# Performance work log

Hardware: AMD Instinct MI355X
Metric: run time of the kernel (lower is better)

The kernel has to match this reference:

```python
import jax, jax.numpy as jnp
import numpy as np

DT_SCALER = 1.0 / 24.0
EULER_STEPS = 10   # odeint euler, t in [0,1], step_size=0.1
STEP = 0.1


def setup_inputs() -> dict:
    key = jax.random.key(0)
    ks = jax.random.split(key, 10)
    B, T, D, H = 8192, 100, 16, 32
    Hd = min((H + D) * 2, 50)  # 50
    x = jax.random.normal(ks[0], (B, T, D), dtype=jnp.float32)
    dt = jax.random.uniform(ks[1], (B, T, 2), dtype=jnp.float32)
    # dh MLP: Linear(H+D -> Hd), tanh, Linear(Hd -> H), tanh ; init N(0, 0.1), bias 0
    W1 = 0.1 * jax.random.normal(ks[2], (Hd, H + D), dtype=jnp.float32)
    b1 = jnp.zeros((Hd,), jnp.float32)
    W2 = 0.1 * jax.random.normal(ks[3], (H, Hd), dtype=jnp.float32)
    b2 = jnp.zeros((H,), jnp.float32)
    # dy MLP: Linear(H -> 2H), tanh, Linear(2H -> 1)
    W3 = 0.1 * jax.random.normal(ks[4], (2 * H, H), dtype=jnp.float32)
    b3 = jnp.zeros((2 * H,), jnp.float32)
    W4 = 0.1 * jax.random.normal(ks[5], (1, 2 * H), dtype=jnp.float32)
    b4 = jnp.zeros((1,), jnp.float32)
    return {"dt": dt, "x": x, "W1": W1, "b1": b1, "W2": W2, "b2": b2,
            "W3": W3, "b3": b3, "W4": W4, "b4": b4}


def _forward(dt, x, W1, b1, W2, b2, W3, b3, W4, b4):
    B, T, D = x.shape
    H = W2.shape[0]
    dti = (dt[:, :, 1] - dt[:, :, 0])[..., None]  # [B,T,1]
    x_t = jnp.swapaxes(x, 0, 1)      # [T,B,D]
    dt_t = jnp.swapaxes(dti, 0, 1)   # [T,B,1]

    def time_step(h, inp):
        x_i, dt_i = inp              # [B,D], [B,1]
        y = x_i[:, 0:1]              # z0 y-part reset to observation each step
        scale = dt_i * DT_SCALER     # [B,1]

        def euler(carry, _):
            y, h = carry
            dh = jnp.tanh(jnp.tanh(jnp.concatenate([x_i, h], axis=1) @ W1.T + b1) @ W2.T + b2) * scale
            dy = (jnp.tanh(h @ W3.T + b3) @ W4.T + b4) * scale
            return (y + STEP * dy, h + STEP * dh), None

        (y, h), _ = jax.lax.scan(euler, (y, h), None, length=EULER_STEPS)
        return h, y

    h0 = jnp.zeros((B, H), jnp.float32)
    _, mu = jax.lax.scan(time_step, h0, (x_t, dt_t))  # mu: [T,B,1]
    return jnp.swapaxes(mu, 0, 1)                     # [B,T,1]


def reference(dt, x, W1, b1, W2, b2, W3, b3, W4, b4):
    return _forward(dt, x, W1, b1, W2, b2, W3, b3, W4, b4)
```

## Files before the change

### kernel.cpp

```cpp
#include <hip/hip_runtime.h>
#include <stdint.h>

#define T_STEPS 100
#define D_IN 16
#define H_DIM 32
#define HD 50
#define KXH 48
#define EULER 10
#define STEPF 0.1f
#define DT_SCALERF (1.0f/24.0f)
#define TANH_SCALE 2.8853900817779268f

typedef __attribute__((ext_vector_type(8))) short short8;
typedef __attribute__((ext_vector_type(4))) float float4v;
typedef __attribute__((ext_vector_type(4))) uint32_t uint4v;

__device__ __forceinline__ float tanh_pre(float us) {
    float e = __builtin_amdgcn_exp2f(us);
    return 1.0f - 2.0f * __builtin_amdgcn_rcpf(e + 1.0f);
}
__device__ __forceinline__ uint32_t pkbf(float lo, float hi) {
    uint32_t r;
    asm("v_cvt_pk_bf16_f32 %0, %1, %2" : "=v"(r) : "v"(lo), "v"(hi));
    return r;
}
__device__ __forceinline__ short f2bf(float f) {
    uint32_t u = __builtin_bit_cast(uint32_t, f);
    u = u + 0x7fffu + ((u >> 16) & 1u);
    return (short)(u >> 16);
}

__device__ __forceinline__ int zorig(int kk) {
    int f = kk >> 5, q = (kk >> 3) & 3, jj = kk & 7;
    int t = 2 * f + (jj >> 2), r = jj & 3;
    if (t < 3) return t * 16 + q * 4 + r;
    if (r == 0 && q < 2) return 48 + q;
    return -1;
}

__global__ __launch_bounds__(128, 1) void latode_kernel(
    const float* __restrict__ dt, const float* __restrict__ x,
    const float* __restrict__ W1, const float* __restrict__ b1,
    const float* __restrict__ W2, const float* __restrict__ b2,
    const float* __restrict__ W3, const float* __restrict__ b3,
    const float* __restrict__ W4, const float* __restrict__ b4,
    float* __restrict__ out)
{
    const int tid  = threadIdx.x;
    const int wave = tid >> 6;
    const int lane = tid & 63;
    const int n16  = lane & 15;
    const int quad = lane >> 4;
    const int b0   = blockIdx.x * 16;

    __shared__ __align__(16) uint32_t hslot[2][256];

    for (int i = tid; i < 512; i += 128) ((uint32_t*)hslot)[i] = 0;

    const float* xrow = x + (size_t)(b0 + n16) * (T_STEPS * D_IN);
    const float* drow = dt + (size_t)(b0 + n16) * (T_STEPS * 2);

    short8 w1h[4], w1x[4], w2f[2][2];
    short8 w3f[4];
    float4v b3v[4], w4v4[4];

    if (wave == 0) {
#pragma unroll
        for (int t = 0; t < 4; ++t) {
            int kz = 32 * (t >> 1) + 8 * (n16 >> 2) + 4 * (t & 1) + (n16 & 3);
            int of = zorig(kz);
#pragma unroll
            for (int j = 0; j < 8; ++j) {
                int kk = quad * 8 + j;
                float wh = 0.0f, wx = 0.0f;
                if (of >= 0) {
                    wh = W1[of * KXH + 16 + kk];
                    if (kk < 16)       wx = W1[of * KXH + kk];
                    else if (kk == 16) wx = b1[of];
                }
                w1h[t][j] = f2bf(wh * TANH_SCALE);
                w1x[t][j] = f2bf(wx * TANH_SCALE);
            }
        }
#pragma unroll
        for (int t2 = 0; t2 < 2; ++t2) {
            int hrow = 8 * (n16 >> 2) + 4 * t2 + (n16 & 3);
#pragma unroll
            for (int kt = 0; kt < 2; ++kt)
#pragma unroll
            for (int j = 0; j < 8; ++j) {
                int kk = kt * 32 + quad * 8 + j;
                int oz = zorig(kk);
                float w = 0.0f;
                if (oz >= 0)       w = W2[hrow * HD + oz];
                else if (kk == 63) w = b2[hrow];
                w2f[t2][kt][j] = f2bf(w * TANH_SCALE);
            }
        }
    } else {
#pragma unroll
        for (int t = 0; t < 4; ++t) {
            int f = t * 16 + n16;
#pragma unroll
            for (int j = 0; j < 8; ++j)
                w3f[t][j] = f2bf(W3[f * H_DIM + quad * 8 + j] * TANH_SCALE);
#pragma unroll
            for (int r = 0; r < 4; ++r) {
                int fr = t * 16 + quad * 4 + r;
                b3v[t][r]  = b3[fr] * TANH_SCALE;
                w4v4[t][r] = W4[fr];
            }
        }
    }
    const float b4s = b4[0];

    const float4v zero4 = {0.f,0.f,0.f,0.f};
    float4v hC0 = zero4, hC1 = zero4;
    short8  hB  = (short8){0,0,0,0,0,0,0,0};
    const uint32_t z1d3 = (quad == 3) ? 0x3f800000u : 0u;

    float4 xa = {0,0,0,0}, xb = {0,0,0,0};
    float2 dtv = {0.f, 0.f};
    float y0 = 0.f;
    if (wave == 0) {
        if (quad < 2) {
            xa = *(const float4*)(xrow + quad * 8);
            xb = *(const float4*)(xrow + quad * 8 + 4);
        }
        dtv = *(const float2*)drow;
    } else {
        dtv = *(const float2*)drow;
        y0  = xrow[0];
    }

    __syncthreads();

#pragma unroll 1
    for (int t = 0; t < T_STEPS; ++t) {
        const float s10 = (dtv.y - dtv.x) * (DT_SCALERF * STEPF);
        const float y0c = y0;
        float psum = 0.f;

        float4v cxa[4];
        if (wave == 0) {
            uint4v xp = {0,0,0,0};
            if (quad < 2) {
                xp[0] = pkbf(xa.x, xa.y); xp[1] = pkbf(xa.z, xa.w);
                xp[2] = pkbf(xb.x, xb.y); xp[3] = pkbf(xb.z, xb.w);
            } else if (quad == 2) {
                xp[0] = 0x00003f80u;
            }
            short8 xB = __builtin_bit_cast(short8, xp);
#pragma unroll
            for (int tt = 0; tt < 4; ++tt)
                cxa[tt] = __builtin_amdgcn_mfma_f32_16x16x32_bf16(w1x[tt], xB, zero4, 0, 0, 0);
        }

        {
            int tn = (t + 1 < T_STEPS) ? t + 1 : (T_STEPS - 1);
            if (wave == 0) {
                if (quad < 2) {
                    xa = *(const float4*)(xrow + tn * D_IN + quad * 8);
                    xb = *(const float4*)(xrow + tn * D_IN + quad * 8 + 4);
                }
                dtv = *(const float2*)(drow + tn * 2);
            } else {
                dtv = *(const float2*)(drow + tn * 2);
                y0  = xrow[tn * D_IN];
            }
        }

#pragma unroll 2
        for (int e = 0; e < EULER; ++e) {
            if (wave == 0) {
                float4v a0 = __builtin_amdgcn_mfma_f32_16x16x32_bf16(w1h[0], hB, cxa[0], 0, 0, 0);
                float4v a1 = __builtin_amdgcn_mfma_f32_16x16x32_bf16(w1h[1], hB, cxa[1], 0, 0, 0);
                float4v a2 = __builtin_amdgcn_mfma_f32_16x16x32_bf16(w1h[2], hB, cxa[2], 0, 0, 0);
                float4v a3 = __builtin_amdgcn_mfma_f32_16x16x32_bf16(w1h[3], hB, cxa[3], 0, 0, 0);
                uint4v z0, z1;
                z0[0] = pkbf(tanh_pre(a0[0]), tanh_pre(a0[1]));
                z0[1] = pkbf(tanh_pre(a0[2]), tanh_pre(a0[3]));
                z0[2] = pkbf(tanh_pre(a1[0]), tanh_pre(a1[1]));
                z0[3] = pkbf(tanh_pre(a1[2]), tanh_pre(a1[3]));
                z1[0] = pkbf(tanh_pre(a2[0]), tanh_pre(a2[1]));
                z1[1] = pkbf(tanh_pre(a2[2]), tanh_pre(a2[3]));
                z1[2] = pkbf(tanh_pre(a3[0]), 0.0f);
                z1[3] = z1d3;
                short8 zf0 = __builtin_bit_cast(short8, z0);
                short8 zf1 = __builtin_bit_cast(short8, z1);
                float4v u20 = __builtin_amdgcn_mfma_f32_16x16x32_bf16(w2f[0][0], zf0, zero4, 0, 0, 0);
                u20 = __builtin_amdgcn_mfma_f32_16x16x32_bf16(w2f[0][1], zf1, u20, 0, 0, 0);
                float4v u21 = __builtin_amdgcn_mfma_f32_16x16x32_bf16(w2f[1][0], zf0, zero4, 0, 0, 0);
                u21 = __builtin_amdgcn_mfma_f32_16x16x32_bf16(w2f[1][1], zf1, u21, 0, 0, 0);
                hC0[0] += s10 * tanh_pre(u20[0]);
                hC0[1] += s10 * tanh_pre(u20[1]);
                hC0[2] += s10 * tanh_pre(u20[2]);
                hC0[3] += s10 * tanh_pre(u20[3]);
                hC1[0] += s10 * tanh_pre(u21[0]);
                hC1[1] += s10 * tanh_pre(u21[1]);
                hC1[2] += s10 * tanh_pre(u21[2]);
                hC1[3] += s10 * tanh_pre(u21[3]);
                uint4v hp;
                hp[0] = pkbf(hC0[0], hC0[1]); hp[1] = pkbf(hC0[2], hC0[3]);
                hp[2] = pkbf(hC1[0], hC1[1]); hp[3] = pkbf(hC1[2], hC1[3]);
                hB = __builtin_bit_cast(short8, hp);
                *(uint4v*)&hslot[(e + 1) & 1][lane * 4] = hp;
            } else {
                short8 hb = __builtin_bit_cast(short8, *(const uint4v*)&hslot[e & 1][lane * 4]);
                float4v c0 = __builtin_amdgcn_mfma_f32_16x16x32_bf16(w3f[0], hb, b3v[0], 0, 0, 0);
                float4v c1 = __builtin_amdgcn_mfma_f32_16x16x32_bf16(w3f[1], hb, b3v[1], 0, 0, 0);
                float4v c2 = __builtin_amdgcn_mfma_f32_16x16x32_bf16(w3f[2], hb, b3v[2], 0, 0, 0);
                float4v c3 = __builtin_amdgcn_mfma_f32_16x16x32_bf16(w3f[3], hb, b3v[3], 0, 0, 0);
                float p0 = w4v4[0][0]*tanh_pre(c0[0]) + w4v4[0][1]*tanh_pre(c0[1])
                         + w4v4[0][2]*tanh_pre(c0[2]) + w4v4[0][3]*tanh_pre(c0[3]);
                float p1 = w4v4[1][0]*tanh_pre(c1[0]) + w4v4[1][1]*tanh_pre(c1[1])
                         + w4v4[1][2]*tanh_pre(c1[2]) + w4v4[1][3]*tanh_pre(c1[3]);
                float p2 = w4v4[2][0]*tanh_pre(c2[0]) + w4v4[2][1]*tanh_pre(c2[1])
                         + w4v4[2][2]*tanh_pre(c2[2]) + w4v4[2][3]*tanh_pre(c2[3]);
                float p3 = w4v4[3][0]*tanh_pre(c3[0]) + w4v4[3][1]*tanh_pre(c3[1])
                         + w4v4[3][2]*tanh_pre(c3[2]) + w4v4[3][3]*tanh_pre(c3[3]);
                psum += (p0 + p1) + (p2 + p3);
            }
            asm volatile("s_waitcnt lgkmcnt(0)" ::: "memory");
            __builtin_amdgcn_s_barrier();
            __builtin_amdgcn_sched_barrier(0);
        }

        if (wave == 1) {
            float pacc = psum;
            pacc += __shfl_xor(pacc, 16, 64);
            pacc += __shfl_xor(pacc, 32, 64);
            if (lane < 16)
                out[(size_t)(b0 + n16) * T_STEPS + t] =
                    y0c + s10 * (pacc + (float)EULER * b4s);
        }
    }
}

extern "C" void kernel_launch(void* const* d_in, const int* in_sizes, int n_in,
                              void* d_out, int out_size, void* d_ws, size_t ws_size,
                              hipStream_t stream) {
    const float* dt = (const float*)d_in[0];
    const float* x  = (const float*)d_in[1];
    const float* W1 = (const float*)d_in[2];
    const float* b1 = (const float*)d_in[3];
    const float* W2 = (const float*)d_in[4];
    const float* b2 = (const float*)d_in[5];
    const float* W3 = (const float*)d_in[6];
    const float* b3 = (const float*)d_in[7];
    const float* W4 = (const float*)d_in[8];
    const float* b4 = (const float*)d_in[9];
    float* out = (float*)d_out;

    const int B = 8192;
    dim3 grid(B / 16), block(128);
    latode_kernel<<<grid, block, 0, stream>>>(dt, x, W1, b1, W2, b2, W3, b3, W4, b4, out);
}
```

Before: 788.5 us.

## Pipeline dy MLP one time step behind dh recurrence via LDS ring buffer

Restructures the two-wave schedule. Wave 0 now runs all 10 Euler steps of the h recurrence without per-step barriers and writes each h state into a double-buffered LDS ring. Wave 1 evaluates the dy MLP for the previous time step from that ring. This replaces ten block barriers per time step with one, which removes the lockstep synchronisation cost. It adds LDS footprint and one extra loop iteration to drain the pipeline.

```diff
diff --git a/kernel.cpp b/kernel.cpp
--- a/kernel.cpp
+++ b/kernel.cpp
@@ -53,9 +53,7 @@
     const int quad = lane >> 4;
     const int b0   = blockIdx.x * 16;
 
-    __shared__ __align__(16) uint32_t hslot[2][256];
-
-    for (int i = tid; i < 512; i += 128) ((uint32_t*)hslot)[i] = 0;
+    __shared__ __align__(16) uint32_t ring[2][EULER][256];
 
     const float* xrow = x + (size_t)(b0 + n16) * (T_STEPS * D_IN);
     const float* drow = dt + (size_t)(b0 + n16) * (T_STEPS * 2);
@@ -117,123 +115,135 @@
     const float4v zero4 = {0.f,0.f,0.f,0.f};
     float4v hC0 = zero4, hC1 = zero4;
     short8  hB  = (short8){0,0,0,0,0,0,0,0};
+    uint4v  hPk = (uint4v){0,0,0,0};
     const uint32_t z1d3 = (quad == 3) ? 0x3f800000u : 0u;
 
     float4 xa = {0,0,0,0}, xb = {0,0,0,0};
-    float2 dtv = {0.f, 0.f};
-    float y0 = 0.f;
+    float2 dtv_p = {0.f,0.f}, dtv_c = {0.f,0.f};
+    float y0_c = 0.f;
     if (wave == 0) {
         if (quad < 2) {
             xa = *(const float4*)(xrow + quad * 8);
             xb = *(const float4*)(xrow + quad * 8 + 4);
         }
-        dtv = *(const float2*)drow;
+        dtv_p = *(const float2*)drow;
     } else {
-        dtv = *(const float2*)drow;
-        y0  = xrow[0];
+        dtv_c = *(const float2*)drow;
+        y0_c  = xrow[0];
     }
 
-    __syncthreads();
-
 #pragma unroll 1
-    for (int t = 0; t < T_STEPS; ++t) {
-        const float s10 = (dtv.y - dtv.x) * (DT_SCALERF * STEPF);
-        const float y0c = y0;
-        float psum = 0.f;
-
-        float4v cxa[4];
+    for (int tau = 0; tau <= T_STEPS; ++tau) {
         if (wave == 0) {
-            uint4v xp = {0,0,0,0};
-            if (quad < 2) {
-                xp[0] = pkbf(xa.x, xa.y); xp[1] = pkbf(xa.z, xa.w);
-                xp[2] = pkbf(xb.x, xb.y); xp[3] = pkbf(xb.z, xb.w);
-            } else if (quad == 2) {
-                xp[0] = 0x00003f80u;
-            }
-            short8 xB = __builtin_bit_cast(short8, xp);
-#pragma unroll
-            for (int tt = 0; tt < 4; ++tt)
-                cxa[tt] = __builtin_amdgcn_mfma_f32_16x16x32_bf16(w1x[tt], xB, zero4, 0, 0, 0);
-        }
-
-        {
-            int tn = (t + 1 < T_STEPS) ? t + 1 : (T_STEPS - 1);
-            if (wave == 0) {
-                if (quad < 2) {
-                    xa = *(const float4*)(xrow + tn * D_IN + quad * 8);
-                    xb = *(const float4*)(xrow + tn * D_IN + quad * 8 + 4);
-                }
-                dtv = *(const float2*)(drow + tn * 2);
-            } else {
-                dtv = *(const float2*)(drow + tn * 2);
-                y0  = xrow[tn * D_IN];
-            }
-        }
-
+            if (tau < T_STEPS) {
+                const float s10 = (dtv_p.y - dtv_p.x) * (DT_SCALERF * STEPF);
+
+                float4v cxa[4];
+                {
+                    uint4v xp = {0,0,0,0};
+                    if (quad < 2) {
+                        xp[0] = pkbf(xa.x, xa.y); xp[1] = pkbf(xa.z, xa.w);
+                        xp[2] = pkbf(xb.x, xb.y); xp[3] = pkbf(xb.z, xb.w);
+                    } else if (quad == 2) {
+                        xp[0] = 0x00003f80u;
+                    }
+                    short8 xB = __builtin_bit_cast(short8, xp);
+#pragma unroll
+                    for (int tt = 0; tt < 4; ++tt)
+                        cxa[tt] = __builtin_amdgcn_mfma_f32_16x16x32_bf16(w1x[tt], xB, zero4, 0, 0, 0);
+                }
+                {
+                    int tn = (tau + 1 < T_STEPS) ? tau + 1 : (T_STEPS - 1);
+                    if (quad < 2) {
+                        xa = *(const float4*)(xrow + tn * D_IN + quad * 8);
+                        xb = *(const float4*)(xrow + tn * D_IN + quad * 8 + 4);
+                    }
+                    dtv_p = *(const float2*)(drow + tn * 2);
+                }
+
+                uint32_t* slot = &ring[tau & 1][0][lane * 4];
 #pragma unroll 2
-        for (int e = 0; e < EULER; ++e) {
-            if (wave == 0) {
-                float4v a0 = __builtin_amdgcn_mfma_f32_16x16x32_bf16(w1h[0], hB, cxa[0], 0, 0, 0);
-                float4v a1 = __builtin_amdgcn_mfma_f32_16x16x32_bf16(w1h[1], hB, cxa[1], 0, 0, 0);
-                float4v a2 = __builtin_amdgcn_mfma_f32_16x16x32_bf16(w1h[2], hB, cxa[2], 0, 0, 0);
-                float4v a3 = __builtin_amdgcn_mfma_f32_16x16x32_bf16(w1h[3], hB, cxa[3], 0, 0, 0);
-                uint4v z0, z1;
-                z0[0] = pkbf(tanh_pre(a0[0]), tanh_pre(a0[1]));
-                z0[1] = pkbf(tanh_pre(a0[2]), tanh_pre(a0[3]));
-                z0[2] = pkbf(tanh_pre(a1[0]), tanh_pre(a1[1]));
-                z0[3] = pkbf(tanh_pre(a1[2]), tanh_pre(a1[3]));
-                z1[0] = pkbf(tanh_pre(a2[0]), tanh_pre(a2[1]));
-                z1[1] = pkbf(tanh_pre(a2[2]), tanh_pre(a2[3]));
-                z1[2] = pkbf(tanh_pre(a3[0]), 0.0f);
-                z1[3] = z1d3;
-                short8 zf0 = __builtin_bit_cast(short8, z0);
-                short8 zf1 = __builtin_bit_cast(short8, z1);
-                float4v u20 = __builtin_amdgcn_mfma_f32_16x16x32_bf16(w2f[0][0], zf0, zero4, 0, 0, 0);
-                u20 = __builtin_amdgcn_mfma_f32_16x16x32_bf16(w2f[0][1], zf1, u20, 0, 0, 0);
-                float4v u21 = __builtin_amdgcn_mfma_f32_16x16x32_bf16(w2f[1][0], zf0, zero4, 0, 0, 0);
-                u21 = __builtin_amdgcn_mfma_f32_16x16x32_bf16(w2f[1][1], zf1, u21, 0, 0, 0);
-                hC0[0] += s10 * tanh_pre(u20[0]);
-                hC0[1] += s10 * tanh_pre(u20[1]);
-                hC0[2] += s10 * tanh_pre(u20[2]);
-                hC0[3] += s10 * tanh_pre(u20[3]);
-                hC1[0] += s10 * tanh_pre(u21[0]);
-                hC1[1] += s10 * tanh_pre(u21[1]);
-                hC1[2] += s10 * tanh_pre(u21[2]);
-                hC1[3] += s10 * tanh_pre(u21[3]);
-                uint4v hp;
-                hp[0] = pkbf(hC0[0], hC0[1]); hp[1] = pkbf(hC0[2], hC0[3]);
-                hp[2] = pkbf(hC1[0], hC1[1]); hp[3] = pkbf(hC1[2], hC1[3]);
-                hB = __builtin_bit_cast(short8, hp);
-                *(uint4v*)&hslot[(e + 1) & 1][lane * 4] = hp;
-            } else {
-                short8 hb = __builtin_bit_cast(short8, *(const uint4v*)&hslot[e & 1][lane * 4]);
-                float4v c0 = __builtin_amdgcn_mfma_f32_16x16x32_bf16(w3f[0], hb, b3v[0], 0, 0, 0);
-                float4v c1 = __builtin_amdgcn_mfma_f32_16x16x32_bf16(w3f[1], hb, b3v[1], 0, 0, 0);
-                float4v c2 = __builtin_amdgcn_mfma_f32_16x16x32_bf16(w3f[2], hb, b3v[2], 0, 0, 0);
-                float4v c3 = __builtin_amdgcn_mfma_f32_16x16x32_bf16(w3f[3], hb, b3v[3], 0, 0, 0);
-                float p0 = w4v4[0][0]*tanh_pre(c0[0]) + w4v4[0][1]*tanh_pre(c0[1])
-                         + w4v4[0][2]*tanh_pre(c0[2]) + w4v4[0][3]*tanh_pre(c0[3]);
-                float p1 = w4v4[1][0]*tanh_pre(c1[0]) + w4v4[1][1]*tanh_pre(c1[1])
-                         + w4v4[1][2]*tanh_pre(c1[2]) + w4v4[1][3]*tanh_pre(c1[3]);
-                float p2 = w4v4[2][0]*tanh_pre(c2[0]) + w4v4[2][1]*tanh_pre(c2[1])
-                         + w4v4[2][2]*tanh_pre(c2[2]) + w4v4[2][3]*tanh_pre(c2[3]);
-                float p3 = w4v4[3][0]*tanh_pre(c3[0]) + w4v4[3][1]*tanh_pre(c3[1])
-                         + w4v4[3][2]*tanh_pre(c3[2]) + w4v4[3][3]*tanh_pre(c3[3]);
-                psum += (p0 + p1) + (p2 + p3);
-            }
-            asm volatile("s_waitcnt lgkmcnt(0)" ::: "memory");
-            __builtin_amdgcn_s_barrier();
-            __builtin_amdgcn_sched_barrier(0);
-        }
-
-        if (wave == 1) {
-            float pacc = psum;
-            pacc += __shfl_xor(pacc, 16, 64);
-            pacc += __shfl_xor(pacc, 32, 64);
-            if (lane < 16)
-                out[(size_t)(b0 + n16) * T_STEPS + t] =
-                    y0c + s10 * (pacc + (float)EULER * b4s);
-        }
+                for (int e = 0; e < EULER; ++e) {
+                    *(uint4v*)(slot + e * 256) = hPk;
+
+                    float4v a0 = __builtin_amdgcn_mfma_f32_16x16x32_bf16(w1h[0], hB, cxa[0], 0, 0, 0);
+                    float4v a1 = __builtin_amdgcn_mfma_f32_16x16x32_bf16(w1h[1], hB, cxa[1], 0, 0, 0);
+                    float4v a2 = __builtin_amdgcn_mfma_f32_16x16x32_bf16(w1h[2], hB, cxa[2], 0, 0, 0);
+                    float4v a3 = __builtin_amdgcn_mfma_f32_16x16x32_bf16(w1h[3], hB, cxa[3], 0, 0, 0);
+                    uint4v z0, z1;
+                    z0[0] = pkbf(tanh_pre(a0[0]), tanh_pre(a0[1]));
+                    z0[1] = pkbf(tanh_pre(a0[2]), tanh_pre(a0[3]));
+                    z0[2] = pkbf(tanh_pre(a1[0]), tanh_pre(a1[1]));
+                    z0[3] = pkbf(tanh_pre(a1[2]), tanh_pre(a1[3]));
+                    z1[0] = pkbf(tanh_pre(a2[0]), tanh_pre(a2[1]));
+                    z1[1] = pkbf(tanh_pre(a2[2]), tanh_pre(a2[3]));
+                    z1[2] = pkbf(tanh_pre(a3[0]), 0.0f);
+                    z1[3] = z1d3;
+                    short8 zf0 = __builtin_bit_cast(short8, z0);
+                    short8 zf1 = __builtin_bit_cast(short8, z1);
+                    float4v u20 = __builtin_amdgcn_mfma_f32_16x16x32_bf16(w2f[0][0], zf0, zero4, 0, 0, 0);
+                    u20 = __builtin_amdgcn_mfma_f32_16x16x32_bf16(w2f[0][1], zf1, u20, 0, 0, 0);
+                    float4v u21 = __builtin_amdgcn_mfma_f32_16x16x32_bf16(w2f[1][0], zf0, zero4, 0, 0, 0);
+                    u21 = __builtin_amdgcn_mfma_f32_16x16x32_bf16(w2f[1][1], zf1, u21, 0, 0, 0);
+                    hC0[0] += s10 * tanh_pre(u20[0]);
+                    hC0[1] += s10 * tanh_pre(u20[1]);
+                    hC0[2] += s10 * tanh_pre(u20[2]);
+                    hC0[3] += s10 * tanh_pre(u20[3]);
+                    hC1[0] += s10 * tanh_pre(u21[0]);
+                    hC1[1] += s10 * tanh_pre(u21[1]);
+                    hC1[2] += s10 * tanh_pre(u21[2]);
+                    hC1[3] += s10 * tanh_pre(u21[3]);
+                    uint4v hp;
+                    hp[0] = pkbf(hC0[0], hC0[1]); hp[1] = pkbf(hC0[2], hC0[3]);
+                    hp[2] = pkbf(hC1[0], hC1[1]); hp[3] = pkbf(hC1[2], hC1[3]);
+                    hPk = hp;
+                    hB  = __builtin_bit_cast(short8, hp);
+                }
+            }
+        } else {
+            if (tau >= 1) {
+                const int t = tau - 1;
+                const float s10 = (dtv_c.y - dtv_c.x) * (DT_SCALERF * STEPF);
+                const float y0c = y0_c;
+                {
+                    int tn = (tau < T_STEPS) ? tau : (T_STEPS - 1);
+                    dtv_c = *(const float2*)(drow + tn * 2);
+                    y0_c  = xrow[tn * D_IN];
+                }
+                const uint32_t* slot = &ring[(tau - 1) & 1][0][lane * 4];
+                uint4v hs[EULER];
+#pragma unroll
+                for (int e = 0; e < EULER; ++e)
+                    hs[e] = *(const uint4v*)(slot + e * 256);
+                float psum = 0.f;
+#pragma unroll
+                for (int e = 0; e < EULER; ++e) {
+                    short8 hb = __builtin_bit_cast(short8, hs[e]);
+                    float4v c0 = __builtin_amdgcn_mfma_f32_16x16x32_bf16(w3f[0], hb, b3v[0], 0, 0, 0);
+                    float4v c1 = __builtin_amdgcn_mfma_f32_16x16x32_bf16(w3f[1], hb, b3v[1], 0, 0, 0);
+                    float4v c2 = __builtin_amdgcn_mfma_f32_16x16x32_bf16(w3f[2], hb, b3v[2], 0, 0, 0);
+                    float4v c3 = __builtin_amdgcn_mfma_f32_16x16x32_bf16(w3f[3], hb, b3v[3], 0, 0, 0);
+                    float p0 = w4v4[0][0]*tanh_pre(c0[0]) + w4v4[0][1]*tanh_pre(c0[1])
+                             + w4v4[0][2]*tanh_pre(c0[2]) + w4v4[0][3]*tanh_pre(c0[3]);
+                    float p1 = w4v4[1][0]*tanh_pre(c1[0]) + w4v4[1][1]*tanh_pre(c1[1])
+                             + w4v4[1][2]*tanh_pre(c1[2]) + w4v4[1][3]*tanh_pre(c1[3]);
+                    float p2 = w4v4[2][0]*tanh_pre(c2[0]) + w4v4[2][1]*tanh_pre(c2[1])
+                             + w4v4[2][2]*tanh_pre(c2[2]) + w4v4[2][3]*tanh_pre(c2[3]);
+                    float p3 = w4v4[3][0]*tanh_pre(c3[0]) + w4v4[3][1]*tanh_pre(c3[1])
+                             + w4v4[3][2]*tanh_pre(c3[2]) + w4v4[3][3]*tanh_pre(c3[3]);
+                    psum += (p0 + p1) + (p2 + p3);
+                }
+                float pacc = psum;
+                pacc += __shfl_xor(pacc, 16, 64);
+                pacc += __shfl_xor(pacc, 32, 64);
+                if (lane < 16)
+                    out[(size_t)(b0 + n16) * T_STEPS + t] =
+                        y0c + s10 * (pacc + (float)EULER * b4s);
+            }
+        }
+        asm volatile("s_waitcnt lgkmcnt(0)" ::: "memory");
+        __builtin_amdgcn_s_barrier();
+        __builtin_amdgcn_sched_barrier(0);
     }
 }
 
```

New measurement: 722.0 us. -8.4%, faster.
